# Kernel optimization log

Measured on AMD Instinct MI355X. Metric: run time of the kernel, lower is better.

The kernel has to match this reference:

```python
import jax, jax.numpy as jnp
import numpy as np

N_HEADS = 16
N_EMBED = 1024
HEAD_DIM = N_EMBED // N_HEADS
B, T = 4, 2048


def setup_inputs() -> dict:
    key = jax.random.key(0)
    k1, k2, k3 = jax.random.split(key, 3)
    scale = 1.0 / np.sqrt(N_EMBED)
    x = jax.random.normal(k1, (B, T, N_EMBED), dtype=jnp.float32)
    w_qkv = jax.random.normal(k2, (N_EMBED, 3 * N_EMBED), dtype=jnp.float32) * scale
    w_out = jax.random.normal(k3, (N_EMBED, N_EMBED), dtype=jnp.float32) * scale
    b_out = jnp.zeros((N_EMBED,), dtype=jnp.float32)
    return {"x": x, "w_qkv": w_qkv, "w_out": w_out, "b_out": b_out}


def reference(x, w_qkv, w_out, b_out):
    b, t, c = x.shape
    # qkv projection (no bias), split into q,k,v per head: [B, H, T, D]
    qkv = (x @ w_qkv).reshape(b, t, 3, N_HEADS, HEAD_DIM)
    q, k, v = jnp.moveaxis(qkv, 2, 0)            # each [B, T, H, D]
    q = jnp.swapaxes(q, 1, 2) * (HEAD_DIM ** -0.5)  # [B, H, T, D]
    k = jnp.swapaxes(k, 1, 2)
    v = jnpp = jnp.swapaxes(v, 1, 2)
    # scores + causal mask
    attn = jnp.einsum('bhqd,bhkd->bhqk', q, k)   # [B, H, T, T]
    causal = jnp.tril(jnp.ones((t, t), dtype=bool))
    attn = jnp.where(causal, attn, -jnp.inf)
    attn = jax.nn.softmax(attn, axis=-1)
    out = jnp.einsum('bhqk,bhkd->bhqd', attn, v)  # [B, H, T, D]
    out = jnp.swapaxes(out, 1, 2).reshape(b, t, c)
    # output projection (dropout is identity in eval mode)
    return out @ w_out + b_out
```

## Files before the change

### kernel.cpp

```cpp
#include <hip/hip_runtime.h>

#define NH 16
#define HD 64
#define CE 1024
#define TT 2048
#define BB 4
#define MM 8192

using bf16x8 = __attribute__((ext_vector_type(8))) __bf16;
using f32x4  = __attribute__((ext_vector_type(4))) float;

__device__ __forceinline__ unsigned short f2bf(float f) {
  unsigned int u = __float_as_uint(f);
  u += 0x7fffu + ((u >> 16) & 1u);
  return (unsigned short)(u >> 16);
}
__device__ __forceinline__ unsigned short f2bf_rtz(float f) {
  return (unsigned short)(__float_as_uint(f) >> 16);
}

__device__ __forceinline__ void async_cp16(const unsigned short* g, unsigned short* l) {
  __builtin_amdgcn_global_load_lds(
      (const __attribute__((address_space(1))) unsigned int*)g,
      (__attribute__((address_space(3))) unsigned int*)l, 16, 0, 0);
}

__global__ __launch_bounds__(256) void prep(const float* __restrict__ x,
                                            const float* __restrict__ w_qkv,
                                            const float* __restrict__ w_out,
                                            unsigned short* __restrict__ Xb,
                                            unsigned short* __restrict__ Wt1,
                                            unsigned short* __restrict__ Wt2) {
  __shared__ unsigned short tile[32][33];
  const int idx = blockIdx.x;
  if (idx < 8192) {
    const int i = (idx * 256 + threadIdx.x) * 4;
    const float4 v = *(const float4*)(x + i);
    ushort4 o;
    o.x = f2bf(v.x); o.y = f2bf(v.y); o.z = f2bf(v.z); o.w = f2bf(v.w);
    *(ushort4*)(Xb + i) = o;
    return;
  }
  const float* in;
  unsigned short* out;
  int rows, cols, bx, by;
  if (idx < 11264) {
    const int tc = idx - 8192;
    in = w_qkv; out = Wt1; rows = 1024; cols = 3072;
    bx = tc % 96; by = tc / 96;
  } else {
    const int tc = idx - 11264;
    in = w_out; out = Wt2; rows = 1024; cols = 1024;
    bx = tc & 31; by = tc >> 5;
  }
  const int c0 = bx * 32, r0 = by * 32;
  const int tx = threadIdx.x & 31, ty = threadIdx.x >> 5;
#pragma unroll
  for (int i = ty; i < 32; i += 8)
    tile[i][tx] = f2bf(in[(size_t)(r0 + i) * cols + c0 + tx]);
  __syncthreads();
#pragma unroll
  for (int i = ty; i < 32; i += 8)
    out[(size_t)(c0 + i) * rows + r0 + tx] = tile[tx][i];
}

__device__ __forceinline__ void gemm_core(const unsigned short* __restrict__ A,
                                          const unsigned short* __restrict__ BT,
                                          int m0, int n0, f32x4 (&acc)[4][4],
                                          unsigned short* As, unsigned short* Bs) {
  const int tid  = threadIdx.x;
  const int lane = tid & 63;
  const int wave = tid >> 6;
  const int quad = lane >> 4;
  const int l15  = lane & 15;
  const int wm = (wave & 1) * 64;
  const int wn = (wave >> 1) * 64;
  const int ldr = tid >> 2;
  const int ldc = (tid & 3) * 8;
  const unsigned short* Ap = A + (size_t)(m0 + ldr) * CE + ldc;
  const unsigned short* Bp = BT + (size_t)(n0 + ldr) * CE + ldc;
  const int wofs = wave * 512;
#define STAGE_K(buf, k0)                                                   \
  do {                                                                     \
    async_cp16(Ap + (k0), As + (buf) * 4096 + wofs);                       \
    async_cp16(Ap + (size_t)64 * CE + (k0), As + (buf) * 4096 + 2048 + wofs); \
    async_cp16(Bp + (k0), Bs + (buf) * 4096 + wofs);                       \
    async_cp16(Bp + (size_t)64 * CE + (k0), Bs + (buf) * 4096 + 2048 + wofs); \
  } while (0)
  STAGE_K(0, 0);
  __syncthreads();
  int cur = 0;
  for (int k0 = 0; k0 < CE; k0 += 32) {
    if (k0 + 32 < CE) STAGE_K(cur ^ 1, k0 + 32);
    const unsigned short* Ab = As + cur * 4096;
    const unsigned short* Bb = Bs + cur * 4096;
    bf16x8 af[4], bfr[4];
#pragma unroll
    for (int i = 0; i < 4; i++) {
      af[i]  = *(const bf16x8*)&Ab[(wm + i * 16 + l15) * 32 + quad * 8];
      bfr[i] = *(const bf16x8*)&Bb[(wn + i * 16 + l15) * 32 + quad * 8];
    }
    __builtin_amdgcn_s_setprio(1);
#pragma unroll
    for (int mi = 0; mi < 4; mi++)
#pragma unroll
      for (int ni = 0; ni < 4; ni++)
        acc[mi][ni] = __builtin_amdgcn_mfma_f32_16x16x32_bf16(af[mi], bfr[ni], acc[mi][ni], 0, 0, 0);
    __builtin_amdgcn_s_setprio(0);
    __syncthreads();
    cur ^= 1;
  }
#undef STAGE_K
}

__global__ __launch_bounds__(256) void gemm_qkv(const unsigned short* __restrict__ A,
                                                const unsigned short* __restrict__ BT,
                                                unsigned short* __restrict__ Qb,
                                                unsigned short* __restrict__ Kb,
                                                unsigned short* __restrict__ Vtb) {
  __shared__ unsigned short pool[16384];
  f32x4 acc[4][4] = {};
  const int m0 = blockIdx.y * 128, n0 = blockIdx.x * 128;
  gemm_core(A, BT, m0, n0, acc, pool, pool + 8192);
  const int tid = threadIdx.x, lane = tid & 63, wave = tid >> 6;
  const int quad = lane >> 4, l15 = lane & 15;
  const int wm = (wave & 1) * 64, wn = (wave >> 1) * 64;
  if (blockIdx.x >= 16) {
    unsigned short* Vt = pool;
    const int h0 = 2 * (blockIdx.x - 16);
    const int bb = m0 >> 11;
    const int t0g = m0 & 2047;
    const int l31 = tid & 31;
    const int rw  = tid >> 5;
    unsigned int* __restrict__ VtU = (unsigned int*)Vtb;
#pragma unroll
    for (int hp = 0; hp < 2; hp++) {
      __syncthreads();
      if ((wave & 1) == hp) {
#pragma unroll
        for (int mi = 0; mi < 4; mi++)
#pragma unroll
          for (int ni = 0; ni < 4; ni++) {
            const int row = wn + ni * 16 + l15;
            const int col = mi * 16 + quad * 4;
#pragma unroll
            for (int r = 0; r < 4; r++)
              Vt[row * 66 + col + r] = f2bf(acc[mi][ni][r]);
          }
      }
      __syncthreads();
#pragma unroll
      for (int k = 0; k < 16; k++) {
        const int d = rw + 8 * k;
        const unsigned int v = *(const unsigned int*)&Vt[d * 66 + 2 * l31];
        const int hh = h0 + (d >> 6);
        VtU[((((size_t)(bb * 16 + hh) * 64 + (d & 63)) * TT + t0g + 64 * hp) >> 1) + l31] = v;
      }
    }
    return;
  }
  const float QSCALE = 0.125f * 1.44269504088896340736f;
#pragma unroll
  for (int mi = 0; mi < 4; mi++) {
#pragma unroll
    for (int ni = 0; ni < 4; ni++) {
      const int n = n0 + wn + ni * 16 + l15;
      const int s = n >> 10;
      const int h = (n >> 6) & 15;
      const int d = n & 63;
#pragma unroll
      for (int r = 0; r < 4; r++) {
        const int m = m0 + wm + mi * 16 + quad * 4 + r;
        const int b = m >> 11;
        const int t = m & 2047;
        const int bh = (b << 4) + h;
        const float v = acc[mi][ni][r];
        if (s == 0) Qb[((size_t)bh * TT + t) * HD + d] = f2bf(v * QSCALE);
        else        Kb[((size_t)bh * TT + t) * HD + d] = f2bf(v);
      }
    }
  }
}

__global__ __launch_bounds__(256) void gemm_out(const unsigned short* __restrict__ A,
                                                const unsigned short* __restrict__ BT,
                                                const float* __restrict__ bias,
                                                float* __restrict__ out) {
  __shared__ unsigned short pool[16384];
  f32x4 acc[4][4] = {};
  const int m0 = blockIdx.y * 128, n0 = blockIdx.x * 128;
  gemm_core(A, BT, m0, n0, acc, pool, pool + 8192);
  const int tid = threadIdx.x, lane = tid & 63, wave = tid >> 6;
  const int quad = lane >> 4, l15 = lane & 15;
  const int wm = (wave & 1) * 64, wn = (wave >> 1) * 64;
#pragma unroll
  for (int mi = 0; mi < 4; mi++) {
#pragma unroll
    for (int ni = 0; ni < 4; ni++) {
      const int n = n0 + wn + ni * 16 + l15;
      const float bv = bias[n];
#pragma unroll
      for (int r = 0; r < 4; r++) {
        const int m = m0 + wm + mi * 16 + quad * 4 + r;
        out[(size_t)m * CE + n] = acc[mi][ni][r] + bv;
      }
    }
  }
}

__global__ __launch_bounds__(512) void flash_attn(const unsigned short* __restrict__ Q,
                                                  const unsigned short* __restrict__ Kg,
                                                  const unsigned short* __restrict__ Vt,
                                                  unsigned short* __restrict__ AO) {
  __shared__ unsigned short Ks[64][72];
  __shared__ unsigned short Vs[64][72];
  __shared__ unsigned short Ps[8][16][72];
  const int flat = blockIdx.x + 8 * blockIdx.y;
  const int wu   = (flat & 7) * 64 + (flat >> 3);
  const int qx   = wu & 7;
  const int bh   = wu >> 3;
  const int tid = threadIdx.x, w = tid >> 6, lane = tid & 63;
  const int quad = lane >> 4, l15 = lane & 15;
  const int b = bh >> 4, h = bh & 15;
  const unsigned short* Kbase = Kg + (size_t)bh * TT * HD;
  const unsigned short* Vbase = Vt + (size_t)bh * HD * TT;
  const int srow = tid >> 3;
  const int scol = (tid & 7) * 8;
  const bf16x8 ones = {1, 1, 1, 1, 1, 1, 1, 1};

  for (int ph = 0; ph < 2; ph++) {
    const int pt = ph ? (15 - qx) : qx;
    const int q0 = pt * 128;
    const int n_it = 2 * pt + 2;
    const int rbase = q0 + w * 16;
    bf16x8 qf[2];
    {
      const unsigned short* Qp =
          Q + ((size_t)bh * TT + rbase + l15) * HD + quad * 8;
      qf[0] = *(const bf16x8*)Qp;
      qf[1] = *(const bf16x8*)(Qp + 32);
    }
    f32x4 o[4] = {};
    f32x4 l_acc = {};
    uint4 kreg, vreg;
    {
      kreg = *(const uint4*)(Kbase + (size_t)srow * HD + scol);
      vreg = *(const uint4*)(Vbase + (size_t)srow * TT + scol);
    }
    for (int it = 0; it < n_it; it++) {
      const int kv0 = it * 64;
      *(uint4*)&Ks[srow][scol] = kreg;
      *(uint4*)&Vs[srow][scol] = vreg;
      {
        const int itn = (it + 1 < n_it) ? it + 1 : it;
        const int kvn = itn * 64;
        kreg = *(const uint4*)(Kbase + (size_t)(kvn + srow) * HD + scol);
        vreg = *(const uint4*)(Vbase + (size_t)srow * TT + kvn + scol);
      }
      __syncthreads();
      if (kv0 <= rbase + 15) {
        bf16x8 kb[4][2];
#pragma unroll
        for (int ni = 0; ni < 4; ni++) {
          kb[ni][0] = *(const bf16x8*)&Ks[ni * 16 + l15][quad * 8];
          kb[ni][1] = *(const bf16x8*)&Ks[ni * 16 + l15][32 + quad * 8];
        }
        f32x4 s[4];
        __builtin_amdgcn_s_setprio(1);
#pragma unroll
        for (int ni = 0; ni < 4; ni++) {
          f32x4 z = {};
          z = __builtin_amdgcn_mfma_f32_16x16x32_bf16(qf[0], kb[ni][0], z, 0, 0, 0);
          z = __builtin_amdgcn_mfma_f32_16x16x32_bf16(qf[1], kb[ni][1], z, 0, 0, 0);
          s[ni] = z;
        }
        __builtin_amdgcn_s_setprio(0);
        if (kv0 + 63 > rbase) {
#pragma unroll
          for (int ni = 0; ni < 4; ni++) {
            const int col_g = kv0 + ni * 16 + l15;
#pragma unroll
            for (int r = 0; r < 4; r++) {
              const int row_g = rbase + quad * 4 + r;
              const float sv = (col_g <= row_g) ? s[ni][r] : -1e30f;
              Ps[w][quad * 4 + r][ni * 16 + l15] = f2bf_rtz(exp2f(sv));
            }
          }
        } else {
#pragma unroll
          for (int ni = 0; ni < 4; ni++)
#pragma unroll
            for (int r = 0; r < 4; r++)
              Ps[w][quad * 4 + r][ni * 16 + l15] = f2bf_rtz(exp2f(s[ni][r]));
        }
        bf16x8 pa[2];
        pa[0] = *(const bf16x8*)&Ps[w][l15][quad * 8];
        pa[1] = *(const bf16x8*)&Ps[w][l15][32 + quad * 8];
        bf16x8 vb[4][2];
#pragma unroll
        for (int nd = 0; nd < 4; nd++) {
          vb[nd][0] = *(const bf16x8*)&Vs[nd * 16 + l15][quad * 8];
          vb[nd][1] = *(const bf16x8*)&Vs[nd * 16 + l15][32 + quad * 8];
        }
        __builtin_amdgcn_s_setprio(1);
        l_acc = __builtin_amdgcn_mfma_f32_16x16x32_bf16(pa[0], ones, l_acc, 0, 0, 0);
        l_acc = __builtin_amdgcn_mfma_f32_16x16x32_bf16(pa[1], ones, l_acc, 0, 0, 0);
#pragma unroll
        for (int nd = 0; nd < 4; nd++) {
          o[nd] = __builtin_amdgcn_mfma_f32_16x16x32_bf16(pa[0], vb[nd][0], o[nd], 0, 0, 0);
          o[nd] = __builtin_amdgcn_mfma_f32_16x16x32_bf16(pa[1], vb[nd][1], o[nd], 0, 0, 0);
        }
        __builtin_amdgcn_s_setprio(0);
      }
      __syncthreads();
    }
    {
      float rin[4];
#pragma unroll
      for (int r = 0; r < 4; r++) rin[r] = __builtin_amdgcn_rcpf(l_acc[r]);
#pragma unroll
      for (int nd = 0; nd < 4; nd++)
#pragma unroll
        for (int r = 0; r < 4; r++) {
          const int row_g = rbase + quad * 4 + r;
          const size_t mg = (size_t)b * TT + row_g;
          AO[mg * CE + h * 64 + nd * 16 + l15] = f2bf(o[nd][r] * rin[r]);
        }
    }
  }
}

extern "C" void kernel_launch(void* const* d_in, const int* in_sizes, int n_in,
                              void* d_out, int out_size, void* d_ws, size_t ws_size,
                              hipStream_t stream) {
  const float* x     = (const float*)d_in[0];
  const float* w_qkv = (const float*)d_in[1];
  const float* w_out = (const float*)d_in[2];
  const float* b_out = (const float*)d_in[3];
  float* out = (float*)d_out;

  unsigned short* ws  = (unsigned short*)d_ws;
  unsigned short* Xb  = ws;
  unsigned short* Wt1 = Xb  + (size_t)MM * CE;
  unsigned short* Wt2 = Wt1 + (size_t)3072 * 1024;
  unsigned short* Qb  = Wt2 + (size_t)1024 * 1024;
  unsigned short* Kb  = Qb  + (size_t)8388608;
  unsigned short* Vtb = Kb  + (size_t)8388608;
  unsigned short* AO  = Vtb + (size_t)8388608;

  prep      <<<dim3(12288), 256, 0, stream>>>(x, w_qkv, w_out, Xb, Wt1, Wt2);
  gemm_qkv  <<<dim3(24, 64), 256, 0, stream>>>(Xb, Wt1, Qb, Kb, Vtb);
  flash_attn<<<dim3(8, 64), 512, 0, stream>>>(Qb, Kb, Vtb, AO);
  gemm_out  <<<dim3(8, 64), 256, 0, stream>>>(AO, Wt2, b_out, out);
}
```

Before: 250.0 us.

## Switch flash attention to 32x32 MFMA with register-resident P via permlane swap

Flash attention now uses 4 waves of 32 query rows each and 32x32x16 bf16 MFMAs instead of 8 waves using 16x16x32 tiles. S is computed transposed (K as the A operand), so each lane's probabilities can be packed with v_cvt_pk_bf16_f32 and redistributed with v_permlane32_swap. That removes the LDS round trip through the Ps buffer. The costs are fewer waves per block, higher register pressure from 16-wide accumulators, and round-to-nearest instead of truncating bf16 conversion.

```diff
diff --git a/kernel.cpp b/kernel.cpp
--- a/kernel.cpp
+++ b/kernel.cpp
@@ -9,14 +9,18 @@
 
 using bf16x8 = __attribute__((ext_vector_type(8))) __bf16;
 using f32x4  = __attribute__((ext_vector_type(4))) float;
+using f32x16 = __attribute__((ext_vector_type(16))) float;
 
 __device__ __forceinline__ unsigned short f2bf(float f) {
   unsigned int u = __float_as_uint(f);
   u += 0x7fffu + ((u >> 16) & 1u);
   return (unsigned short)(u >> 16);
 }
-__device__ __forceinline__ unsigned short f2bf_rtz(float f) {
-  return (unsigned short)(__float_as_uint(f) >> 16);
+
+__device__ __forceinline__ unsigned cvtpk(float lo, float hi) {
+  unsigned r;
+  asm("v_cvt_pk_bf16_f32 %0, %1, %2" : "=v"(r) : "v"(lo), "v"(hi));
+  return r;
 }
 
 __device__ __forceinline__ void async_cp16(const unsigned short* g, unsigned short* l) {
@@ -208,124 +212,124 @@
   }
 }
 
-__global__ __launch_bounds__(512) void flash_attn(const unsigned short* __restrict__ Q,
+__global__ __launch_bounds__(256) void flash_attn(const unsigned short* __restrict__ Q,
                                                   const unsigned short* __restrict__ Kg,
                                                   const unsigned short* __restrict__ Vt,
                                                   unsigned short* __restrict__ AO) {
   __shared__ unsigned short Ks[64][72];
   __shared__ unsigned short Vs[64][72];
-  __shared__ unsigned short Ps[8][16][72];
   const int flat = blockIdx.x + 8 * blockIdx.y;
   const int wu   = (flat & 7) * 64 + (flat >> 3);
   const int qx   = wu & 7;
   const int bh   = wu >> 3;
   const int tid = threadIdx.x, w = tid >> 6, lane = tid & 63;
-  const int quad = lane >> 4, l15 = lane & 15;
+  const int l31 = lane & 31, hi = lane >> 5;
   const int b = bh >> 4, h = bh & 15;
   const unsigned short* Kbase = Kg + (size_t)bh * TT * HD;
   const unsigned short* Vbase = Vt + (size_t)bh * HD * TT;
-  const int srow = tid >> 3;
-  const int scol = (tid & 7) * 8;
+  const int srow = tid >> 2;
+  const int scol = (tid & 3) * 16;
   const bf16x8 ones = {1, 1, 1, 1, 1, 1, 1, 1};
 
   for (int ph = 0; ph < 2; ph++) {
     const int pt = ph ? (15 - qx) : qx;
     const int q0 = pt * 128;
     const int n_it = 2 * pt + 2;
-    const int rbase = q0 + w * 16;
-    bf16x8 qf[2];
+    const int wr = q0 + w * 32;
+    bf16x8 qf[4];
+#pragma unroll
+    for (int ds_ = 0; ds_ < 4; ds_++)
+      qf[ds_] = *(const bf16x8*)(Q + ((size_t)bh * TT + wr + l31) * HD + ds_ * 16 + hi * 8);
+    f32x16 o0 = {}, o1 = {}, l_acc = {};
+    uint4 kreg[2], vreg[2];
     {
-      const unsigned short* Qp =
-          Q + ((size_t)bh * TT + rbase + l15) * HD + quad * 8;
-      qf[0] = *(const bf16x8*)Qp;
-      qf[1] = *(const bf16x8*)(Qp + 32);
-    }
-    f32x4 o[4] = {};
-    f32x4 l_acc = {};
-    uint4 kreg, vreg;
-    {
-      kreg = *(const uint4*)(Kbase + (size_t)srow * HD + scol);
-      vreg = *(const uint4*)(Vbase + (size_t)srow * TT + scol);
+      const unsigned short* kp = Kbase + (size_t)srow * HD + scol;
+      kreg[0] = *(const uint4*)kp;
+      kreg[1] = *(const uint4*)(kp + 8);
+      const unsigned short* vp = Vbase + (size_t)srow * TT + scol;
+      vreg[0] = *(const uint4*)vp;
+      vreg[1] = *(const uint4*)(vp + 8);
     }
     for (int it = 0; it < n_it; it++) {
       const int kv0 = it * 64;
-      *(uint4*)&Ks[srow][scol] = kreg;
-      *(uint4*)&Vs[srow][scol] = vreg;
+      *(uint4*)&Ks[srow][scol]     = kreg[0];
+      *(uint4*)&Ks[srow][scol + 8] = kreg[1];
+      *(uint4*)&Vs[srow][scol]     = vreg[0];
+      *(uint4*)&Vs[srow][scol + 8] = vreg[1];
       {
         const int itn = (it + 1 < n_it) ? it + 1 : it;
         const int kvn = itn * 64;
-        kreg = *(const uint4*)(Kbase + (size_t)(kvn + srow) * HD + scol);
-        vreg = *(const uint4*)(Vbase + (size_t)srow * TT + kvn + scol);
+        const unsigned short* kp = Kbase + (size_t)(kvn + srow) * HD + scol;
+        kreg[0] = *(const uint4*)kp;
+        kreg[1] = *(const uint4*)(kp + 8);
+        const unsigned short* vp = Vbase + (size_t)srow * TT + kvn + scol;
+        vreg[0] = *(const uint4*)vp;
+        vreg[1] = *(const uint4*)(vp + 8);
       }
       __syncthreads();
-      if (kv0 <= rbase + 15) {
-        bf16x8 kb[4][2];
-#pragma unroll
-        for (int ni = 0; ni < 4; ni++) {
-          kb[ni][0] = *(const bf16x8*)&Ks[ni * 16 + l15][quad * 8];
-          kb[ni][1] = *(const bf16x8*)&Ks[ni * 16 + l15][32 + quad * 8];
+      if (kv0 <= wr + 31) {
+        const int qg = wr + l31;
+#pragma unroll
+        for (int kt = 0; kt < 2; kt++) {
+          f32x16 sc = {};
+          __builtin_amdgcn_s_setprio(1);
+#pragma unroll
+          for (int ds_ = 0; ds_ < 4; ds_++) {
+            const bf16x8 kb = *(const bf16x8*)&Ks[kt * 32 + l31][ds_ * 16 + hi * 8];
+            sc = __builtin_amdgcn_mfma_f32_32x32x16_bf16(kb, qf[ds_], sc, 0, 0, 0);
+          }
+          __builtin_amdgcn_s_setprio(0);
+          float p[16];
+          const int kvb = kv0 + kt * 32 + 4 * hi;
+          if (kv0 + 63 > wr) {
+#pragma unroll
+            for (int r = 0; r < 16; r++) {
+              const int kvg = kvb + (r & 3) + 8 * (r >> 2);
+              p[r] = exp2f(kvg <= qg ? sc[r] : -1e30f);
+            }
+          } else {
+#pragma unroll
+            for (int r = 0; r < 16; r++) p[r] = exp2f(sc[r]);
+          }
+          bf16x8 pa[2];
+#pragma unroll
+          for (int sl = 0; sl < 2; sl++) {
+            unsigned a0 = cvtpk(p[8 * sl + 0], p[8 * sl + 1]);
+            unsigned a1 = cvtpk(p[8 * sl + 2], p[8 * sl + 3]);
+            unsigned a2 = cvtpk(p[8 * sl + 4], p[8 * sl + 5]);
+            unsigned a3 = cvtpk(p[8 * sl + 6], p[8 * sl + 7]);
+            asm volatile("v_permlane32_swap_b32 %0, %1" : "+v"(a0), "+v"(a2));
+            asm volatile("v_permlane32_swap_b32 %0, %1" : "+v"(a1), "+v"(a3));
+            union { unsigned u[4]; bf16x8 v; } c;
+            c.u[0] = a0; c.u[1] = a1; c.u[2] = a2; c.u[3] = a3;
+            pa[sl] = c.v;
+          }
+          __builtin_amdgcn_s_setprio(1);
+          l_acc = __builtin_amdgcn_mfma_f32_32x32x16_bf16(pa[0], ones, l_acc, 0, 0, 0);
+          l_acc = __builtin_amdgcn_mfma_f32_32x32x16_bf16(pa[1], ones, l_acc, 0, 0, 0);
+#pragma unroll
+          for (int sl = 0; sl < 2; sl++) {
+            const bf16x8 vb0 = *(const bf16x8*)&Vs[l31][kt * 32 + sl * 16 + hi * 8];
+            const bf16x8 vb1 = *(const bf16x8*)&Vs[32 + l31][kt * 32 + sl * 16 + hi * 8];
+            o0 = __builtin_amdgcn_mfma_f32_32x32x16_bf16(pa[sl], vb0, o0, 0, 0, 0);
+            o1 = __builtin_amdgcn_mfma_f32_32x32x16_bf16(pa[sl], vb1, o1, 0, 0, 0);
+          }
+          __builtin_amdgcn_s_setprio(0);
         }
-        f32x4 s[4];
-        __builtin_amdgcn_s_setprio(1);
-#pragma unroll
-        for (int ni = 0; ni < 4; ni++) {
-          f32x4 z = {};
-          z = __builtin_amdgcn_mfma_f32_16x16x32_bf16(qf[0], kb[ni][0], z, 0, 0, 0);
-          z = __builtin_amdgcn_mfma_f32_16x16x32_bf16(qf[1], kb[ni][1], z, 0, 0, 0);
-          s[ni] = z;
-        }
-        __builtin_amdgcn_s_setprio(0);
-        if (kv0 + 63 > rbase) {
-#pragma unroll
-          for (int ni = 0; ni < 4; ni++) {
-            const int col_g = kv0 + ni * 16 + l15;
-#pragma unroll
-            for (int r = 0; r < 4; r++) {
-              const int row_g = rbase + quad * 4 + r;
-              const float sv = (col_g <= row_g) ? s[ni][r] : -1e30f;
-              Ps[w][quad * 4 + r][ni * 16 + l15] = f2bf_rtz(exp2f(sv));
-            }
-          }
-        } else {
-#pragma unroll
-          for (int ni = 0; ni < 4; ni++)
-#pragma unroll
-            for (int r = 0; r < 4; r++)
-              Ps[w][quad * 4 + r][ni * 16 + l15] = f2bf_rtz(exp2f(s[ni][r]));
-        }
-        bf16x8 pa[2];
-        pa[0] = *(const bf16x8*)&Ps[w][l15][quad * 8];
-        pa[1] = *(const bf16x8*)&Ps[w][l15][32 + quad * 8];
-        bf16x8 vb[4][2];
-#pragma unroll
-        for (int nd = 0; nd < 4; nd++) {
-          vb[nd][0] = *(const bf16x8*)&Vs[nd * 16 + l15][quad * 8];
-          vb[nd][1] = *(const bf16x8*)&Vs[nd * 16 + l15][32 + quad * 8];
-        }
-        __builtin_amdgcn_s_setprio(1);
-        l_acc = __builtin_amdgcn_mfma_f32_16x16x32_bf16(pa[0], ones, l_acc, 0, 0, 0);
-        l_acc = __builtin_amdgcn_mfma_f32_16x16x32_bf16(pa[1], ones, l_acc, 0, 0, 0);
-#pragma unroll
-        for (int nd = 0; nd < 4; nd++) {
-          o[nd] = __builtin_amdgcn_mfma_f32_16x16x32_bf16(pa[0], vb[nd][0], o[nd], 0, 0, 0);
-          o[nd] = __builtin_amdgcn_mfma_f32_16x16x32_bf16(pa[1], vb[nd][1], o[nd], 0, 0, 0);
-        }
-        __builtin_amdgcn_s_setprio(0);
       }
       __syncthreads();
     }
     {
-      float rin[4];
-#pragma unroll
-      for (int r = 0; r < 4; r++) rin[r] = __builtin_amdgcn_rcpf(l_acc[r]);
-#pragma unroll
-      for (int nd = 0; nd < 4; nd++)
-#pragma unroll
-        for (int r = 0; r < 4; r++) {
-          const int row_g = rbase + quad * 4 + r;
-          const size_t mg = (size_t)b * TT + row_g;
-          AO[mg * CE + h * 64 + nd * 16 + l15] = f2bf(o[nd][r] * rin[r]);
-        }
+      float rin[16];
+#pragma unroll
+      for (int r = 0; r < 16; r++) rin[r] = __builtin_amdgcn_rcpf(l_acc[r]);
+#pragma unroll
+      for (int r = 0; r < 16; r++) {
+        const int row_g = wr + (r & 3) + 8 * (r >> 2) + 4 * hi;
+        const size_t base = ((size_t)b * TT + row_g) * CE + h * 64;
+        AO[base + l31]      = f2bf(o0[r] * rin[r]);
+        AO[base + 32 + l31] = f2bf(o1[r] * rin[r]);
+      }
     }
   }
 }
@@ -350,6 +354,6 @@
 
   prep      <<<dim3(12288), 256, 0, stream>>>(x, w_qkv, w_out, Xb, Wt1, Wt2);
   gemm_qkv  <<<dim3(24, 64), 256, 0, stream>>>(Xb, Wt1, Qb, Kb, Vtb);
-  flash_attn<<<dim3(8, 64), 512, 0, stream>>>(Qb, Kb, Vtb, AO);
+  flash_attn<<<dim3(8, 64), 256, 0, stream>>>(Qb, Kb, Vtb, AO);
   gemm_out  <<<dim3(8, 64), 256, 0, stream>>>(AO, Wt2, b_out, out);
 }
```

After: 287.4 us. +15.0%, slower.
